# Kernel optimization log

Measured on AMD Instinct MI355X. Metric: run time of the kernel, lower is better.

Reference implementation:

```python
import jax, jax.numpy as jnp
import numpy as np

TOP_K = 2


def setup_inputs() -> dict:
    key = jax.random.key(0)
    k1, k2, k3, k4 = jax.random.split(key, 4)
    B, S, H, I, E = 8, 2048, 768, 3072, 8
    x = jax.random.normal(k1, (B, S, H), dtype=jnp.float32)
    # kaiming_uniform-ish scale for weights
    router_w = jax.random.uniform(k2, (E, H), dtype=jnp.float32, minval=-1.0, maxval=1.0) * (1.0 / np.sqrt(H))
    up_w = jax.random.uniform(k3, (E, H, I), dtype=jnp.float32, minval=-1.0, maxval=1.0) * (1.0 / np.sqrt(H))
    down_w = jax.random.uniform(k4, (E, I, H), dtype=jnp.float32, minval=-1.0, maxval=1.0) * (1.0 / np.sqrt(I))
    return {"x": x, "router_w": router_w, "up_w": up_w, "down_w": down_w}


def reference(x, router_w, up_w, down_w):
    B, S, H = x.shape
    E = up_w.shape[0]
    T = B * S
    xf = x.reshape(T, H)
    # router: Linear(H -> E, bias=False) then softmax, top-k, renormalize
    logits = xf @ router_w.T                      # [T, E]
    probs = jax.nn.softmax(logits, axis=-1)
    top_w, top_i = jax.lax.top_k(probs, TOP_K)    # [T, K]
    top_w = top_w / jnp.sum(top_w, axis=-1, keepdims=True)
    # dense per-(token, expert) gate: zero for unselected experts
    gate = jnp.zeros((T, E), dtype=xf.dtype).at[jnp.arange(T)[:, None], top_i].add(top_w)
    # combine: sum_e gate[:, e] * down_e(gelu(up_e(x)))
    out = jnp.zeros_like(xf)
    for e in range(E):  # fixed small expert count; loop is structural, not over data dims
        h = jax.nn.gelu(xf @ up_w[e], approximate=False)   # exact GELU == torch F.gelu
        out = out + gate[:, e:e + 1] * (h @ down_w[e])
    return out.reshape(B, S, H)
```

## Files before the change

kernel.cpp:

```cpp
#include <hip/hip_runtime.h>

typedef short bf16x8 __attribute__((ext_vector_type(8)));
typedef float f32x4  __attribute__((ext_vector_type(4)));

#define T_TOK 16384
#define HD 768
#define ID 3072
#define NE 8
#define NT1MAX 136

__device__ __forceinline__ unsigned short f2bf(float f) {
    unsigned int u = __float_as_uint(f);
    unsigned int r = (u + 0x7FFFu + ((u >> 16) & 1u)) >> 16;
    return (unsigned short)r;
}

__device__ __forceinline__ void gload16(const void* g, void* l) {
    __builtin_amdgcn_global_load_lds(
        (const __attribute__((address_space(1))) void*)g,
        (__attribute__((address_space(3))) void*)l, 16, 0, 0);
}

__device__ __forceinline__ float gelu_f(float x) {
    float z = fabsf(x) * 0.70710678118f;
    float t = 1.0f / fmaf(0.3275911f, z, 1.0f);
    float p = t * fmaf(t, fmaf(t, fmaf(t, fmaf(t, 1.061405429f, -1.453152027f),
                                       1.421413741f), -0.284496736f), 0.254829592f);
    float e = 1.0f - p * __expf(-z * z);
    float erfv = (x >= 0.f) ? e : -e;
    return 0.5f * x * (1.0f + erfv);
}

__global__ __launch_bounds__(256) void k_cvt_x(const float* __restrict__ x,
                                               unsigned short* __restrict__ xb) {
    int i = blockIdx.x * 256 + threadIdx.x;
    float4 v = ((const float4*)x)[i];
    ushort4 o;
    o.x = f2bf(v.x); o.y = f2bf(v.y); o.z = f2bf(v.z); o.w = f2bf(v.w);
    ((ushort4*)xb)[i] = o;
}

__global__ __launch_bounds__(256) void k_tp(const float* __restrict__ in,
                                            unsigned short* __restrict__ out,
                                            int R, int C) {
    __shared__ float t[64][65];
    const float* ine = in + (size_t)blockIdx.z * R * C;
    unsigned short* oute = out + (size_t)blockIdx.z * R * C;
    int c0 = blockIdx.x * 64, r0 = blockIdx.y * 64;
    int lc = threadIdx.x & 63, lr4 = threadIdx.x >> 6;
#pragma unroll
    for (int i = 0; i < 16; i++) {
        int r = i * 4 + lr4;
        t[r][lc] = ine[(size_t)(r0 + r) * C + c0 + lc];
    }
    __syncthreads();
#pragma unroll
    for (int i = 0; i < 16; i++) {
        int r = i * 4 + lr4;
        oute[(size_t)(c0 + r) * R + r0 + lc] = f2bf(t[lc][r]);
    }
}

__global__ __launch_bounds__(256) void k_router(const float* __restrict__ x,
                                                const float* __restrict__ rw,
                                                int* __restrict__ topE,
                                                float* __restrict__ topW) {
    __shared__ float lrw[NE * HD];
    for (int i = threadIdx.x; i < NE * HD; i += 256) lrw[i] = rw[i];
    __syncthreads();
    int lane = threadIdx.x & 63;
    int t = blockIdx.x * 4 + (threadIdx.x >> 6);
    const float* xr = x + (size_t)t * HD;
    float acc[NE] = {0, 0, 0, 0, 0, 0, 0, 0};
    for (int h = lane; h < HD; h += 64) {
        float xv = xr[h];
#pragma unroll
        for (int e = 0; e < NE; e++) acc[e] = fmaf(xv, lrw[e * HD + h], acc[e]);
    }
#pragma unroll
    for (int e = 0; e < NE; e++) {
        float v = acc[e];
#pragma unroll
        for (int o = 32; o > 0; o >>= 1) v += __shfl_xor(v, o, 64);
        acc[e] = v;
    }
    if (lane == 0) {
        int e1 = 0; float l1 = acc[0];
#pragma unroll
        for (int e = 1; e < NE; e++) if (acc[e] > l1) { l1 = acc[e]; e1 = e; }
        int e2 = -1; float l2 = -1e30f;
#pragma unroll
        for (int e = 0; e < NE; e++) if (e != e1 && acc[e] > l2) { l2 = acc[e]; e2 = e; }
        float ex = expf(l2 - l1);
        float w1 = 1.0f / (1.0f + ex);
        topE[2 * t] = e1; topE[2 * t + 1] = e2;
        topW[2 * t] = w1; topW[2 * t + 1] = ex * w1;
    }
}

__global__ __launch_bounds__(256) void k_scatter(const int* __restrict__ topE,
                                                 const float* __restrict__ topW,
                                                 int* __restrict__ counts,
                                                 int* __restrict__ tokL,
                                                 float* __restrict__ gateL) {
    __shared__ int lc[NE], lbase[NE];
    if (threadIdx.x < NE) lc[threadIdx.x] = 0;
    __syncthreads();
    int t = blockIdx.x * 256 + threadIdx.x;
    int e1 = topE[2 * t], e2 = topE[2 * t + 1];
    int p1 = atomicAdd(&lc[e1], 1);
    int p2 = atomicAdd(&lc[e2], 1);
    __syncthreads();
    if (threadIdx.x < NE) lbase[threadIdx.x] = atomicAdd(&counts[threadIdx.x], lc[threadIdx.x]);
    __syncthreads();
    int q1 = lbase[e1] + p1, q2 = lbase[e2] + p2;
    tokL[e1 * T_TOK + q1] = t;  gateL[e1 * T_TOK + q1] = topW[2 * t];
    tokL[e2 * T_TOK + q2] = t;  gateL[e2 * T_TOK + q2] = topW[2 * t + 1];
}

__global__ void k_desc(const int* __restrict__ counts, int* __restrict__ tileE,
                       int* __restrict__ tileM0, int* __restrict__ tileHB) {
    if (threadIdx.x == 0 && blockIdx.x == 0) {
        int off = 0, tl = 0;
        for (int e = 0; e < NE; e++) {
            int c = counts[e];
            int nt = (c + 255) >> 8;
            for (int t = 0; t < nt; t++) {
                tileE[tl] = e; tileM0[tl] = t << 8; tileHB[tl] = off + (t << 8); tl++;
            }
            off += c;
        }
        for (; tl < NT1MAX; tl++) { tileE[tl] = -1; tileM0[tl] = 0; tileHB[tl] = 0; }
    }
}

__global__ __launch_bounds__(512, 2) void k_gemm1(
    const unsigned short* __restrict__ xb,
    const unsigned short* __restrict__ upt,
    const int* __restrict__ tokL,
    const int* __restrict__ counts,
    const int* __restrict__ tileE,
    const int* __restrict__ tileM0,
    const int* __restrict__ tileHB,
    unsigned short* __restrict__ h) {
    __shared__ __align__(16) char lds[4][32768];
    constexpr int NK = HD / 32;
    constexpr int NWG = NT1MAX * 12;
    int bid = blockIdx.x;
    int L = (bid & 7) * (NWG >> 3) + (bid >> 3);
    int mt = L / 12, nt = L - mt * 12;
    int e = tileE[mt];
    if (e < 0) return;
    int m0 = tileM0[mt];
    int hb = tileHB[mt];
    int nrow = min(256, counts[e] - m0);
    const int* tok = tokL + e * T_TOK + m0;
    int n0 = nt * 256;

    const int tid = threadIdx.x, lane = tid & 63, wid = tid >> 6;
    const int wm = wid >> 2, wn = wid & 3;
    const int g = lane >> 4, r = lane & 15;

    int ar0 = wid * 16 + r;
    int ar1 = 128 + wid * 16 + r;
    const char* a0 = (const char*)(xb + (size_t)tok[ar0 < nrow ? ar0 : 0] * HD);
    const char* a1 = (const char*)(xb + (size_t)tok[ar1 < nrow ? ar1 : 0] * HD);
    const char* bsl = (const char*)(upt + (size_t)e * ID * HD);
    const char* b0 = bsl + (size_t)(n0 + wid * 16 + r) * (HD * 2);
    const char* b1 = bsl + (size_t)(n0 + 128 + wid * 16 + r) * (HD * 2);
    const int dstoff = wid * 1024 + lane * 16;
    const int koff = g * 16;

    auto issue = [&](int step, int slot) {
        char* base = &lds[slot][0];
        int kb = step * 64 + koff;
        gload16(a0 + kb, base + dstoff);
        gload16(a1 + kb, base + 8192 + dstoff);
        gload16(b0 + kb, base + 16384 + dstoff);
        gload16(b1 + kb, base + 24576 + dstoff);
    };

    f32x4 acc[8][4];
#pragma unroll
    for (int m = 0; m < 8; m++)
#pragma unroll
        for (int n = 0; n < 4; n++) acc[m][n] = (f32x4){0.f, 0.f, 0.f, 0.f};

    issue(0, 0); issue(1, 1); issue(2, 2);
    asm volatile("s_waitcnt vmcnt(8)" ::: "memory");
    __builtin_amdgcn_s_barrier();
    asm volatile("" ::: "memory");

    const int aoff = wm * 8192 + g * 256 + r * 16;
    const int boff = 16384 + wn * 4096 + g * 256 + r * 16;

    for (int k = 0; k < NK; k++) {
        char* base = &lds[k & 3][0];
        bf16x8 a[4], b[4];
#pragma unroll
        for (int n = 0; n < 4; n++) b[n] = *(const bf16x8*)(base + boff + n * 1024);
#pragma unroll
        for (int m = 0; m < 4; m++) a[m] = *(const bf16x8*)(base + aoff + m * 1024);
        issue(min(k + 3, NK - 1), (k + 3) & 3);
        __builtin_amdgcn_s_setprio(1);
#pragma unroll
        for (int m = 0; m < 4; m++)
#pragma unroll
            for (int n = 0; n < 4; n++)
                acc[m][n] = __builtin_amdgcn_mfma_f32_16x16x32_bf16(a[m], b[n], acc[m][n], 0, 0, 0);
        __builtin_amdgcn_s_setprio(0);
#pragma unroll
        for (int m = 0; m < 4; m++) a[m] = *(const bf16x8*)(base + aoff + (4 + m) * 1024);
        __builtin_amdgcn_s_setprio(1);
#pragma unroll
        for (int m = 0; m < 4; m++)
#pragma unroll
            for (int n = 0; n < 4; n++)
                acc[4 + m][n] = __builtin_amdgcn_mfma_f32_16x16x32_bf16(a[m], b[n], acc[4 + m][n], 0, 0, 0);
        __builtin_amdgcn_s_setprio(0);
        asm volatile("s_waitcnt vmcnt(8)" ::: "memory");
        __builtin_amdgcn_s_barrier();
        asm volatile("" ::: "memory");
    }
    asm volatile("s_waitcnt vmcnt(0)" ::: "memory");

#pragma unroll
    for (int m = 0; m < 8; m++)
#pragma unroll
        for (int j = 0; j < 4; j++) {
            int rl = wm * 128 + m * 16 + g * 4 + j;
            if (rl < nrow) {
                unsigned short* hr = h + (size_t)(hb + rl) * ID + n0 + wn * 64 + r;
#pragma unroll
                for (int n = 0; n < 4; n++) hr[n * 16] = f2bf(gelu_f(acc[m][n][j]));
            }
        }
}

__global__ __launch_bounds__(512, 2) void k_gemm2(
    const unsigned short* __restrict__ h,
    const unsigned short* __restrict__ dnt,
    const int* __restrict__ tokL,
    const float* __restrict__ gateL,
    const int* __restrict__ counts,
    const int* __restrict__ tileE,
    const int* __restrict__ tileM0,
    const int* __restrict__ tileHB,
    float* __restrict__ out) {
    __shared__ __align__(16) char lds[4][32768];
    constexpr int NK = ID / 32;
    constexpr int NWG = NT1MAX * 3;
    int bid = blockIdx.x;
    int L = (bid & 7) * (NWG >> 3) + (bid >> 3);
    int mt = L / 3, nt = L - mt * 3;
    int e = tileE[mt];
    if (e < 0) return;
    int m0 = tileM0[mt];
    int hb = tileHB[mt];
    int nrow = min(256, counts[e] - m0);
    const int* tok = tokL + e * T_TOK + m0;
    const float* gat = gateL + e * T_TOK + m0;
    int n0 = nt * 256;

    const int tid = threadIdx.x, lane = tid & 63, wid = tid >> 6;
    const int wm = wid >> 2, wn = wid & 3;
    const int g = lane >> 4, r = lane & 15;

    int ar0 = wid * 16 + r;
    int ar1 = 128 + wid * 16 + r;
    const char* a0 = (const char*)(h + (size_t)(hb + ar0) * ID);
    const char* a1 = (const char*)(h + (size_t)(hb + ar1) * ID);
    const char* bsl = (const char*)(dnt + (size_t)e * ID * HD);
    const char* b0 = bsl + (size_t)(n0 + wid * 16 + r) * (ID * 2);
    const char* b1 = bsl + (size_t)(n0 + 128 + wid * 16 + r) * (ID * 2);
    const int dstoff = wid * 1024 + lane * 16;
    const int koff = g * 16;

    auto issue = [&](int step, int slot) {
        char* base = &lds[slot][0];
        int kb = step * 64 + koff;
        gload16(a0 + kb, base + dstoff);
        gload16(a1 + kb, base + 8192 + dstoff);
        gload16(b0 + kb, base + 16384 + dstoff);
        gload16(b1 + kb, base + 24576 + dstoff);
    };

    f32x4 acc[8][4];
#pragma unroll
    for (int m = 0; m < 8; m++)
#pragma unroll
        for (int n = 0; n < 4; n++) acc[m][n] = (f32x4){0.f, 0.f, 0.f, 0.f};

    issue(0, 0); issue(1, 1); issue(2, 2);
    asm volatile("s_waitcnt vmcnt(8)" ::: "memory");
    __builtin_amdgcn_s_barrier();
    asm volatile("" ::: "memory");

    const int aoff = wm * 8192 + g * 256 + r * 16;
    const int boff = 16384 + wn * 4096 + g * 256 + r * 16;

    for (int k = 0; k < NK; k++) {
        char* base = &lds[k & 3][0];
        bf16x8 a[4], b[4];
#pragma unroll
        for (int n = 0; n < 4; n++) b[n] = *(const bf16x8*)(base + boff + n * 1024);
#pragma unroll
        for (int m = 0; m < 4; m++) a[m] = *(const bf16x8*)(base + aoff + m * 1024);
        issue(min(k + 3, NK - 1), (k + 3) & 3);
        __builtin_amdgcn_s_setprio(1);
#pragma unroll
        for (int m = 0; m < 4; m++)
#pragma unroll
            for (int n = 0; n < 4; n++)
                acc[m][n] = __builtin_amdgcn_mfma_f32_16x16x32_bf16(a[m], b[n], acc[m][n], 0, 0, 0);
        __builtin_amdgcn_s_setprio(0);
#pragma unroll
        for (int m = 0; m < 4; m++) a[m] = *(const bf16x8*)(base + aoff + (4 + m) * 1024);
        __builtin_amdgcn_s_setprio(1);
#pragma unroll
        for (int m = 0; m < 4; m++)
#pragma unroll
            for (int n = 0; n < 4; n++)
                acc[4 + m][n] = __builtin_amdgcn_mfma_f32_16x16x32_bf16(a[m], b[n], acc[4 + m][n], 0, 0, 0);
        __builtin_amdgcn_s_setprio(0);
        asm volatile("s_waitcnt vmcnt(8)" ::: "memory");
        __builtin_amdgcn_s_barrier();
        asm volatile("" ::: "memory");
    }
    asm volatile("s_waitcnt vmcnt(0)" ::: "memory");

#pragma unroll
    for (int m = 0; m < 8; m++)
#pragma unroll
        for (int j = 0; j < 4; j++) {
            int rl = wm * 128 + m * 16 + g * 4 + j;
            if (rl < nrow) {
                int t = tok[rl];
                float gv = gat[rl];
                float* orow = out + (size_t)t * HD + n0 + wn * 64 + r;
#pragma unroll
                for (int n = 0; n < 4; n++)
                    atomicAdd(orow + n * 16, gv * acc[m][n][j]);
            }
        }
}

__global__ __launch_bounds__(512, 2) void k_moe(
    const unsigned short* __restrict__ xb,
    const unsigned short* __restrict__ upt,
    const unsigned short* __restrict__ dnt,
    const int* __restrict__ counts,
    const int* __restrict__ tokL,
    const float* __restrict__ gateL,
    float* __restrict__ out) {
    __shared__ __align__(16) char lds[155648];
    char* xs = lds;
    char* hs = lds + 98304;
    char* ring = lds + 106496;

    const int e = blockIdx.x & 7;
    const int slot = blockIdx.x >> 3;
    const int cnt = counts[e];
    if (slot * 64 >= cnt) return;
    const int nrow = min(64, cnt - slot * 64);
    const int* tok = tokL + e * T_TOK + slot * 64;
    const float* gat = gateL + e * T_TOK + slot * 64;

    const int tid = threadIdx.x;
    const int lane = tid & 63;
    const int wid = tid >> 6;
    const int mi = wid >> 2, ni = wid & 3;

    const char* upe = (const char*)(upt + (size_t)e * ID * HD);
    const char* dne = (const char*)(dnt + (size_t)e * HD * ID);

    {
        int off = tid * 16;
#pragma unroll
        for (int s = 0; s < 12; s++) {
            int o = off + s * 8192;
            int m = o / 1536;
            int cb = o - m * 1536;
            int tk = (m < nrow) ? tok[m] : tok[0];
            const char* src = (const char*)xb + (size_t)tk * 1536 + (size_t)(cb ^ ((m & 7) << 4));
            gload16(src, xs + s * 8192 + wid * 1024);
        }
    }
    asm volatile("s_waitcnt vmcnt(0)" ::: "memory");
    __builtin_amdgcn_s_barrier();
    asm volatile("" ::: "memory");

    auto issue = [&](int s) {
        char* dst = ring + (s % 6) * 8192 + wid * 1024;
        int ci = s / 24;
        int ph = s - ci * 24;
        int row = tid >> 3;
        int cb = (tid & 7) << 4;
        int scb = cb ^ ((row & 7) << 4);
        const char* src;
        if (ci >= 48) src = upe;
        else if (ph < 12) src = upe + (size_t)(ci * 64 + row) * 1536 + ph * 128 + scb;
        else              src = dne + (size_t)((ph - 12) * 64 + row) * 6144 + ci * 128 + scb;
        gload16(src, dst);
    };

    f32x4 acc[2][12];
#pragma unroll
    for (int a = 0; a < 2; a++)
#pragma unroll
        for (int b = 0; b < 12; b++) acc[a][b] = (f32x4){0.f, 0.f, 0.f, 0.f};

    issue(0); issue(1); issue(2); issue(3);

    f32x4 acch[2];
    bf16x8 ha[2][2];

    for (int ci = 0; ci < 48; ci++) {
#pragma unroll
        for (int ks = 0; ks < 12; ks++) {
            issue(ci * 24 + ks + 4);
            asm volatile("s_waitcnt vmcnt(4)" ::: "memory");
            __builtin_amdgcn_s_barrier();
            asm volatile("" ::: "memory");
            char* buf = ring + (ks % 6) * 8192;
            if (ks == 0) { acch[0] = (f32x4){0.f,0.f,0.f,0.f}; acch[1] = (f32x4){0.f,0.f,0.f,0.f}; }
#pragma unroll
            for (int kr = 0; kr < 2; kr++) {
                int bn = ni * 16 + (lane & 15);
                int bo = ((kr * 32 + (lane >> 4) * 8) * 2) ^ ((bn & 7) << 4);
                bf16x8 bfrag = *(const bf16x8*)(buf + bn * 128 + bo);
#pragma unroll
                for (int mr = 0; mr < 2; mr++) {
                    int ar = mi * 32 + mr * 16 + (lane & 15);
                    int ao = ((ks * 64 + kr * 32 + (lane >> 4) * 8) * 2) ^ ((ar & 7) << 4);
                    bf16x8 afrag = *(const bf16x8*)(xs + ar * 1536 + ao);
                    acch[mr] = __builtin_amdgcn_mfma_f32_16x16x32_bf16(afrag, bfrag, acch[mr], 0, 0, 0);
                }
            }
            if (ks == 11) {
#pragma unroll
                for (int mr = 0; mr < 2; mr++) {
                    int col = ni * 16 + (lane & 15);
#pragma unroll
                    for (int r = 0; r < 4; r++) {
                        int m = mi * 32 + mr * 16 + (lane >> 4) * 4 + r;
                        float v = acch[mr][r];
                        *(unsigned short*)(hs + m * 128 + ((col * 2) ^ ((m & 7) << 4))) = f2bf(gelu_f(v));
                    }
                }
                asm volatile("s_waitcnt lgkmcnt(0)" ::: "memory");
            }
        }
#pragma unroll
        for (int j = 0; j < 12; j++) {
            issue(ci * 24 + 12 + j + 4);
            asm volatile("s_waitcnt vmcnt(4)" ::: "memory");
            __builtin_amdgcn_s_barrier();
            asm volatile("" ::: "memory");
            char* buf = ring + ((12 + j) % 6) * 8192;
            if (j == 0) {
#pragma unroll
                for (int mr = 0; mr < 2; mr++)
#pragma unroll
                    for (int kr = 0; kr < 2; kr++) {
                        int ar = mi * 32 + mr * 16 + (lane & 15);
                        int ao = ((kr * 32 + (lane >> 4) * 8) * 2) ^ ((ar & 7) << 4);
                        ha[mr][kr] = *(const bf16x8*)(hs + ar * 128 + ao);
                    }
            }
#pragma unroll
            for (int kr = 0; kr < 2; kr++) {
                int bn = ni * 16 + (lane & 15);
                int bo = ((kr * 32 + (lane >> 4) * 8) * 2) ^ ((bn & 7) << 4);
                bf16x8 bfrag = *(const bf16x8*)(buf + bn * 128 + bo);
#pragma unroll
                for (int mr = 0; mr < 2; mr++)
                    acc[mr][j] = __builtin_amdgcn_mfma_f32_16x16x32_bf16(ha[mr][kr], bfrag, acc[mr][j], 0, 0, 0);
            }
        }
    }

    int   t4[2][4];
    float g4[2][4];
#pragma unroll
    for (int mr = 0; mr < 2; mr++)
#pragma unroll
        for (int r = 0; r < 4; r++) {
            int m = mi * 32 + mr * 16 + (lane >> 4) * 4 + r;
            bool valid = m < nrow;
            t4[mr][r] = valid ? tok[m] : -1;
            g4[mr][r] = valid ? gat[m] : 0.f;
        }
#pragma unroll
    for (int mr = 0; mr < 2; mr++)
#pragma unroll
        for (int j = 0; j < 12; j++) {
            int colg = j * 64 + ni * 16 + (lane & 15);
#pragma unroll
            for (int r = 0; r < 4; r++) {
                if (t4[mr][r] >= 0)
                    atomicAdd(out + (size_t)t4[mr][r] * HD + colg, g4[mr][r] * acc[mr][j][r]);
            }
        }
}

extern "C" void kernel_launch(void* const* d_in, const int* in_sizes, int n_in,
                              void* d_out, int out_size, void* d_ws, size_t ws_size,
                              hipStream_t stream) {
    const float* x  = (const float*)d_in[0];
    const float* rw = (const float*)d_in[1];
    const float* uw = (const float*)d_in[2];
    const float* dw = (const float*)d_in[3];
    float* out = (float*)d_out;

    size_t off = 0;
    char* base = (char*)d_ws;
    auto alloc = [&](size_t bytes) -> char* {
        char* p = base + off;
        off += (bytes + 1023) & ~(size_t)1023;
        return p;
    };
    unsigned short* xb   = (unsigned short*)alloc((size_t)T_TOK * HD * 2);
    unsigned short* upt  = (unsigned short*)alloc((size_t)NE * ID * HD * 2);
    unsigned short* dnt  = (unsigned short*)alloc((size_t)NE * HD * ID * 2);
    int*   topE   = (int*)alloc((size_t)T_TOK * 2 * 4);
    float* topW   = (float*)alloc((size_t)T_TOK * 2 * 4);
    int*   counts = (int*)alloc(256);
    int*   tileE  = (int*)alloc(NT1MAX * 4);
    int*   tileM0 = (int*)alloc(NT1MAX * 4);
    int*   tileHB = (int*)alloc(NT1MAX * 4);
    int*   tokL   = (int*)alloc((size_t)NE * T_TOK * 4);
    float* gateL  = (float*)alloc((size_t)NE * T_TOK * 4);
    unsigned short* h = (unsigned short*)alloc((size_t)(T_TOK * 2 + 256) * ID * 2);
    size_t need = off;

    hipMemsetAsync(d_out, 0, (size_t)T_TOK * HD * 4, stream);
    hipMemsetAsync(counts, 0, 256, stream);

    k_cvt_x<<<(T_TOK * HD) / (256 * 4), 256, 0, stream>>>(x, xb);
    k_tp<<<dim3(ID / 64, HD / 64, NE), 256, 0, stream>>>(uw, upt, HD, ID);
    k_tp<<<dim3(HD / 64, ID / 64, NE), 256, 0, stream>>>(dw, dnt, ID, HD);
    k_router<<<T_TOK / 4, 256, 0, stream>>>(x, rw, topE, topW);
    k_scatter<<<T_TOK / 256, 256, 0, stream>>>(topE, topW, counts, tokL, gateL);

    if (ws_size >= need) {
        k_desc<<<1, 64, 0, stream>>>(counts, tileE, tileM0, tileHB);
        k_gemm1<<<NT1MAX * 12, 512, 0, stream>>>(xb, upt, tokL, counts, tileE, tileM0, tileHB, h);
        k_gemm2<<<NT1MAX * 3, 512, 0, stream>>>(h, dnt, tokL, gateL, counts, tileE, tileM0, tileHB, out);
    } else {
        k_moe<<<2048, 512, 0, stream>>>(xb, upt, dnt, counts, tokL, gateL, out);
    }
}
```

Measured before the change: 770.2 us.

## Split intermediate dimension into segments so the two-GEMM path fits workspace

The intermediate dimension is split into S segments, chosen as the smallest count whose per-tile padded h buffer fits the workspace. Each segment runs gemm1 on a slice of up_w columns, then gemm2 over the matching K-slice of down_w, accumulating into out. This lets the tiled two-GEMM path run when the workspace is too small for the full h buffer, instead of falling back to the fused k_moe kernel. It also adds an XCD swizzle helper that handles grid sizes not divisible by 8, and it drops the compact tileHB offsets in favour of padded per-tile row indexing. The cost is extra kernel launches, repeated reads of x and accumulation traffic into out across segments.

```diff
diff --git a/kernel.cpp b/kernel.cpp
--- a/kernel.cpp
+++ b/kernel.cpp
@@ -29,6 +29,12 @@
     float e = 1.0f - p * __expf(-z * z);
     float erfv = (x >= 0.f) ? e : -e;
     return 0.5f * x * (1.0f + erfv);
+}
+
+__device__ __forceinline__ int xcd_swz(int bid, int nwg) {
+    int q = nwg >> 3, rr = nwg & 7;
+    int xcd = bid & 7, seq = bid >> 3;
+    return (xcd < rr ? xcd * (q + 1) : rr * (q + 1) + (xcd - rr) * q) + seq;
 }
 
 __global__ __launch_bounds__(256) void k_cvt_x(const float* __restrict__ x,
@@ -119,18 +125,15 @@
 }
 
 __global__ void k_desc(const int* __restrict__ counts, int* __restrict__ tileE,
-                       int* __restrict__ tileM0, int* __restrict__ tileHB) {
+                       int* __restrict__ tileM0) {
     if (threadIdx.x == 0 && blockIdx.x == 0) {
-        int off = 0, tl = 0;
+        int tl = 0;
         for (int e = 0; e < NE; e++) {
             int c = counts[e];
             int nt = (c + 255) >> 8;
-            for (int t = 0; t < nt; t++) {
-                tileE[tl] = e; tileM0[tl] = t << 8; tileHB[tl] = off + (t << 8); tl++;
-            }
-            off += c;
-        }
-        for (; tl < NT1MAX; tl++) { tileE[tl] = -1; tileM0[tl] = 0; tileHB[tl] = 0; }
+            for (int t = 0; t < nt; t++) { tileE[tl] = e; tileM0[tl] = t << 8; tl++; }
+        }
+        for (; tl < NT1MAX; tl++) { tileE[tl] = -1; tileM0[tl] = 0; }
     }
 }
 
@@ -141,21 +144,18 @@
     const int* __restrict__ counts,
     const int* __restrict__ tileE,
     const int* __restrict__ tileM0,
-    const int* __restrict__ tileHB,
-    unsigned short* __restrict__ h) {
+    unsigned short* __restrict__ h,
+    int seg, int ntn, int ldh) {
     __shared__ __align__(16) char lds[4][32768];
     constexpr int NK = HD / 32;
-    constexpr int NWG = NT1MAX * 12;
-    int bid = blockIdx.x;
-    int L = (bid & 7) * (NWG >> 3) + (bid >> 3);
-    int mt = L / 12, nt = L - mt * 12;
+    int L = xcd_swz(blockIdx.x, gridDim.x);
+    int mt = L / ntn, ntl = L - mt * ntn;
     int e = tileE[mt];
     if (e < 0) return;
     int m0 = tileM0[mt];
-    int hb = tileHB[mt];
     int nrow = min(256, counts[e] - m0);
     const int* tok = tokL + e * T_TOK + m0;
-    int n0 = nt * 256;
+    int n0 = (seg * ntn + ntl) * 256;
 
     const int tid = threadIdx.x, lane = tid & 63, wid = tid >> 6;
     const int wm = wid >> 2, wn = wid & 3;
@@ -168,16 +168,16 @@
     const char* bsl = (const char*)(upt + (size_t)e * ID * HD);
     const char* b0 = bsl + (size_t)(n0 + wid * 16 + r) * (HD * 2);
     const char* b1 = bsl + (size_t)(n0 + 128 + wid * 16 + r) * (HD * 2);
-    const int dstoff = wid * 1024 + lane * 16;
+    const int dst = wid * 1024;
     const int koff = g * 16;
 
     auto issue = [&](int step, int slot) {
         char* base = &lds[slot][0];
         int kb = step * 64 + koff;
-        gload16(a0 + kb, base + dstoff);
-        gload16(a1 + kb, base + 8192 + dstoff);
-        gload16(b0 + kb, base + 16384 + dstoff);
-        gload16(b1 + kb, base + 24576 + dstoff);
+        gload16(a0 + kb, base + dst);
+        gload16(a1 + kb, base + 8192 + dst);
+        gload16(b0 + kb, base + 16384 + dst);
+        gload16(b1 + kb, base + 24576 + dst);
     };
 
     f32x4 acc[8][4];
@@ -230,7 +230,7 @@
         for (int j = 0; j < 4; j++) {
             int rl = wm * 128 + m * 16 + g * 4 + j;
             if (rl < nrow) {
-                unsigned short* hr = h + (size_t)(hb + rl) * ID + n0 + wn * 64 + r;
+                unsigned short* hr = h + (size_t)(mt * 256 + rl) * ldh + ntl * 256 + wn * 64 + r;
 #pragma unroll
                 for (int n = 0; n < 4; n++) hr[n * 16] = f2bf(gelu_f(acc[m][n][j]));
             }
@@ -245,22 +245,18 @@
     const int* __restrict__ counts,
     const int* __restrict__ tileE,
     const int* __restrict__ tileM0,
-    const int* __restrict__ tileHB,
-    float* __restrict__ out) {
+    float* __restrict__ out,
+    int seg, int ldh, int nk) {
     __shared__ __align__(16) char lds[4][32768];
-    constexpr int NK = ID / 32;
-    constexpr int NWG = NT1MAX * 3;
-    int bid = blockIdx.x;
-    int L = (bid & 7) * (NWG >> 3) + (bid >> 3);
-    int mt = L / 3, nt = L - mt * 3;
+    int L = xcd_swz(blockIdx.x, gridDim.x);
+    int mt = L / 3, ntl = L - mt * 3;
     int e = tileE[mt];
     if (e < 0) return;
     int m0 = tileM0[mt];
-    int hb = tileHB[mt];
     int nrow = min(256, counts[e] - m0);
     const int* tok = tokL + e * T_TOK + m0;
     const float* gat = gateL + e * T_TOK + m0;
-    int n0 = nt * 256;
+    int n0 = ntl * 256;
 
     const int tid = threadIdx.x, lane = tid & 63, wid = tid >> 6;
     const int wm = wid >> 2, wn = wid & 3;
@@ -268,21 +264,21 @@
 
     int ar0 = wid * 16 + r;
     int ar1 = 128 + wid * 16 + r;
-    const char* a0 = (const char*)(h + (size_t)(hb + ar0) * ID);
-    const char* a1 = (const char*)(h + (size_t)(hb + ar1) * ID);
-    const char* bsl = (const char*)(dnt + (size_t)e * ID * HD);
+    const char* a0 = (const char*)h + ((size_t)(mt * 256 + ar0) * ldh) * 2;
+    const char* a1 = (const char*)h + ((size_t)(mt * 256 + ar1) * ldh) * 2;
+    const char* bsl = (const char*)(dnt + (size_t)e * ID * HD) + (size_t)seg * ldh * 2;
     const char* b0 = bsl + (size_t)(n0 + wid * 16 + r) * (ID * 2);
     const char* b1 = bsl + (size_t)(n0 + 128 + wid * 16 + r) * (ID * 2);
-    const int dstoff = wid * 1024 + lane * 16;
+    const int dst = wid * 1024;
     const int koff = g * 16;
 
     auto issue = [&](int step, int slot) {
         char* base = &lds[slot][0];
         int kb = step * 64 + koff;
-        gload16(a0 + kb, base + dstoff);
-        gload16(a1 + kb, base + 8192 + dstoff);
-        gload16(b0 + kb, base + 16384 + dstoff);
-        gload16(b1 + kb, base + 24576 + dstoff);
+        gload16(a0 + kb, base + dst);
+        gload16(a1 + kb, base + 8192 + dst);
+        gload16(b0 + kb, base + 16384 + dst);
+        gload16(b1 + kb, base + 24576 + dst);
     };
 
     f32x4 acc[8][4];
@@ -299,14 +295,14 @@
     const int aoff = wm * 8192 + g * 256 + r * 16;
     const int boff = 16384 + wn * 4096 + g * 256 + r * 16;
 
-    for (int k = 0; k < NK; k++) {
+    for (int k = 0; k < nk; k++) {
         char* base = &lds[k & 3][0];
         bf16x8 a[4], b[4];
 #pragma unroll
         for (int n = 0; n < 4; n++) b[n] = *(const bf16x8*)(base + boff + n * 1024);
 #pragma unroll
         for (int m = 0; m < 4; m++) a[m] = *(const bf16x8*)(base + aoff + m * 1024);
-        issue(min(k + 3, NK - 1), (k + 3) & 3);
+        issue(min(k + 3, nk - 1), (k + 3) & 3);
         __builtin_amdgcn_s_setprio(1);
 #pragma unroll
         for (int m = 0; m < 4; m++)
@@ -528,11 +524,18 @@
     int*   counts = (int*)alloc(256);
     int*   tileE  = (int*)alloc(NT1MAX * 4);
     int*   tileM0 = (int*)alloc(NT1MAX * 4);
-    int*   tileHB = (int*)alloc(NT1MAX * 4);
     int*   tokL   = (int*)alloc((size_t)NE * T_TOK * 4);
     float* gateL  = (float*)alloc((size_t)NE * T_TOK * 4);
-    unsigned short* h = (unsigned short*)alloc((size_t)(T_TOK * 2 + 256) * ID * 2);
-    size_t need = off;
+    size_t fixed = off;
+
+    const int cand[6] = {1, 2, 3, 4, 6, 12};
+    int S = 0;
+    size_t hrows = (size_t)NT1MAX * 256;
+    for (int i = 0; i < 6; i++) {
+        size_t hb = hrows * (ID / cand[i]) * 2;
+        if (fixed + hb <= ws_size) { S = cand[i]; break; }
+    }
+    unsigned short* h = (unsigned short*)(base + fixed);
 
     hipMemsetAsync(d_out, 0, (size_t)T_TOK * HD * 4, stream);
     hipMemsetAsync(counts, 0, 256, stream);
@@ -543,10 +546,17 @@
     k_router<<<T_TOK / 4, 256, 0, stream>>>(x, rw, topE, topW);
     k_scatter<<<T_TOK / 256, 256, 0, stream>>>(topE, topW, counts, tokL, gateL);
 
-    if (ws_size >= need) {
-        k_desc<<<1, 64, 0, stream>>>(counts, tileE, tileM0, tileHB);
-        k_gemm1<<<NT1MAX * 12, 512, 0, stream>>>(xb, upt, tokL, counts, tileE, tileM0, tileHB, h);
-        k_gemm2<<<NT1MAX * 3, 512, 0, stream>>>(h, dnt, tokL, gateL, counts, tileE, tileM0, tileHB, out);
+    if (S > 0) {
+        int ntn = 12 / S;
+        int ldh = ID / S;
+        int nk2 = ldh / 32;
+        k_desc<<<1, 64, 0, stream>>>(counts, tileE, tileM0);
+        for (int sg = 0; sg < S; sg++) {
+            k_gemm1<<<NT1MAX * ntn, 512, 0, stream>>>(xb, upt, tokL, counts, tileE, tileM0,
+                                                      h, sg, ntn, ldh);
+            k_gemm2<<<NT1MAX * 3, 512, 0, stream>>>(h, dnt, tokL, gateL, counts, tileE, tileM0,
+                                                    out, sg, ldh, nk2);
+        }
     } else {
         k_moe<<<2048, 512, 0, stream>>>(xb, upt, dnt, counts, tokL, gateL, out);
     }
```

New measurement: 775.6 us. Within noise of the previous version (+0.7%).
